# Optimization experiments

Hardware: AMD Instinct MI355X
Metric: run time of the kernel (lower is better)

## Reference

```python
import jax, jax.numpy as jnp
import numpy as np

L, H, E, V, BS = 12, 12, 768, 50257, 1024
HS = E // H
EPS = 1e-5


def _ln(x, w, b):
    m = jnp.mean(x, axis=-1, keepdims=True)
    v = jnp.mean(jnp.square(x - m), axis=-1, keepdims=True)
    return (x - m) * jax.lax.rsqrt(v + EPS) * w + b


def setup_inputs() -> dict:
    key = jax.random.key(0)
    ks = jax.random.split(key, 16)
    s = 0.02
    inp = {
        "idx": jax.random.randint(ks[0], (2, 1024), 0, V),
        "wte": jax.random.normal(ks[1], (V, E), jnp.float32) * s,
        "wpe": jax.random.normal(ks[2], (BS, E), jnp.float32) * s,
        "ln1_w": jnp.ones((L, E), jnp.float32),
        "ln1_b": jnp.zeros((L, E), jnp.float32),
        "attn_w": jax.random.normal(ks[3], (L, E, 3 * E), jnp.float32) * s,
        "attn_b": jnp.zeros((L, 3 * E), jnp.float32),
        "proj_w": jax.random.normal(ks[4], (L, E, E), jnp.float32) * s,
        "proj_b": jnp.zeros((L, E), jnp.float32),
        "ln2_w": jnp.ones((L, E), jnp.float32),
        "ln2_b": jnp.zeros((L, E), jnp.float32),
        "fc_w": jax.random.normal(ks[5], (L, E, 4 * E), jnp.float32) * s,
        "fc_b": jnp.zeros((L, 4 * E), jnp.float32),
        "fcp_w": jax.random.normal(ks[6], (L, 4 * E, E), jnp.float32) * s,
        "fcp_b": jnp.zeros((L, E), jnp.float32),
        "lnf_w": jnp.ones((E,), jnp.float32),
        "lnf_b": jnp.zeros((E,), jnp.float32),
    }
    return inp


def _gpt_forward(idx, wte, wpe, ln1_w, ln1_b, attn_w, attn_b, proj_w, proj_b,
                 ln2_w, ln2_b, fc_w, fc_b, fcp_w, fcp_b, lnf_w, lnf_b):
    B, T = idx.shape
    x = wte[idx] + wpe[:T]  # [B,T,E]
    causal = jnp.tril(jnp.ones((T, T), bool))
    scale = 1.0 / np.sqrt(HS)

    def block(x, p):
        (l1w, l1b, aw, ab, pw, pb, l2w, l2b, fw, fb, pww, pwb) = p
        qkv = _ln(x, l1w, l1b) @ aw + ab  # [B,T,3E]
        q, k, v = jnp.split(qkv, 3, axis=-1)
        q = q.reshape(B, T, H, HS).transpose(0, 2, 1, 3)  # [B,H,T,hs]
        k = k.reshape(B, T, H, HS).transpose(0, 2, 1, 3)
        v = v.reshape(B, T, H, HS).transpose(0, 2, 1, 3)
        att = jnp.einsum('bhqd,bhkd->bhqk', q, k) * scale
        att = jnp.where(causal, att, -jnp.inf)
        att = jax.nn.softmax(att, axis=-1)
        y = jnp.einsum('bhqk,bhkd->bhqd', att, v)
        y = y.transpose(0, 2, 1, 3).reshape(B, T, E)
        x = x + y @ pw + pb
        h = jax.nn.gelu(_ln(x, l2w, l2b) @ fw + fb, approximate=False)
        x = x + h @ pww + pwb
        return x, None

    params = (ln1_w, ln1_b, attn_w, attn_b, proj_w, proj_b,
              ln2_w, ln2_b, fc_w, fc_b, fcp_w, fcp_b)
    x, _ = jax.lax.scan(block, x, params)
    x = _ln(x, lnf_w, lnf_b)
    return x @ wte.T  # tied lm_head, training-mode full logits [B,T,V]


def reference(idx, wte, wpe, ln1_w, ln1_b, attn_w, attn_b, proj_w, proj_b,
              ln2_w, ln2_b, fc_w, fc_b, fcp_w, fcp_b, lnf_w, lnf_b):
    return _gpt_forward(idx, wte, wpe, ln1_w, ln1_b, attn_w, attn_b, proj_w,
                        proj_b, ln2_w, ln2_b, fc_w, fc_b, fcp_w, fcp_b,
                        lnf_w, lnf_b)
```

## Files before the change

kernel.cpp:

```cpp
#include <hip/hip_runtime.h>
#include <hip/hip_bf16.h>


typedef __bf16 bf16x8 __attribute__((ext_vector_type(8)));
typedef float f32x4 __attribute__((ext_vector_type(4)));
typedef unsigned int u32x4 __attribute__((ext_vector_type(4)));
typedef unsigned short ushort_t;

__device__ inline unsigned short f2bf(float f) {
    unsigned int u = __float_as_uint(f);
    u += 0x7FFFu + ((u >> 16) & 1u);
    return (unsigned short)(u >> 16);
}
__device__ inline unsigned int pk2(float a, float b) {
    return (unsigned int)f2bf(a) | ((unsigned int)f2bf(b) << 16);
}
__device__ inline float gelu_f(float v) {
    return 0.5f * v * (1.0f + erff(v * 0.70710678118654752f));
}
__device__ inline void gld16(const ushort_t* g, ushort_t* l) {
    __builtin_amdgcn_global_load_lds(
        (const __attribute__((address_space(1))) void*)g,
        (__attribute__((address_space(3))) void*)l, 16, 0, 0);
}
__device__ inline void store_c(float* p, float v) { *p = v; }
__device__ inline void store_c(ushort_t* p, float v) { *p = f2bf(v); }

__global__ __launch_bounds__(192) void embed_kernel(
    const int* __restrict__ idx, const float* __restrict__ wte,
    const float* __restrict__ wpe, float* __restrict__ x) {
    int row = blockIdx.x;
    int t = row & 1023;
    int tok = idx[row];
    const float4* src = (const float4*)(wte + (size_t)tok * 768);
    const float4* pe  = (const float4*)(wpe + (size_t)t * 768);
    float4* dst = (float4*)(x + (size_t)row * 768);
    int i = threadIdx.x;
    float4 a = src[i], b = pe[i];
    float4 r; r.x = a.x + b.x; r.y = a.y + b.y; r.z = a.z + b.z; r.w = a.w + b.w;
    dst[i] = r;
}

__global__ __launch_bounds__(256) void ln_kernel(
    const float* __restrict__ in, const float* __restrict__ w,
    const float* __restrict__ b, ushort_t* __restrict__ out) {
    int row = blockIdx.x;
    const float* r = in + (size_t)row * 768;
    int tid = threadIdx.x;
    float v[3];
#pragma unroll
    for (int j = 0; j < 3; j++) v[j] = r[tid + j * 256];
    float s = v[0] + v[1] + v[2];
    __shared__ float sh1[4], sh2[4];
#pragma unroll
    for (int o = 32; o; o >>= 1) s += __shfl_down(s, o);
    if ((tid & 63) == 0) sh1[tid >> 6] = s;
    __syncthreads();
    float mean = (sh1[0] + sh1[1] + sh1[2] + sh1[3]) * (1.0f / 768.0f);
    float d0 = v[0] - mean, d1 = v[1] - mean, d2 = v[2] - mean;
    float sq = d0 * d0 + d1 * d1 + d2 * d2;
#pragma unroll
    for (int o = 32; o; o >>= 1) sq += __shfl_down(sq, o);
    if ((tid & 63) == 0) sh2[tid >> 6] = sq;
    __syncthreads();
    float var = (sh2[0] + sh2[1] + sh2[2] + sh2[3]) * (1.0f / 768.0f);
    float rstd = rsqrtf(var + 1e-5f);
#pragma unroll
    for (int j = 0; j < 3; j++) {
        int c = tid + j * 256;
        out[(size_t)row * 768 + c] = f2bf((v[j] - mean) * rstd * w[c] + b[c]);
    }
}

__global__ __launch_bounds__(256) void transpose_all(
    const float* __restrict__ aw, const float* __restrict__ pw,
    const float* __restrict__ fw, const float* __restrict__ fpw,
    ushort_t* __restrict__ awT, ushort_t* __restrict__ pwT,
    ushort_t* __restrict__ fwT, ushort_t* __restrict__ fpwT) {
    int t = blockIdx.x;
    const float* in; ushort_t* out; int N, K, n0, k0;
    if (t < 432)       { in = aw;  out = awT;  N = 2304; K = 768;
                         n0 = (t % 36) * 64; k0 = (t / 36) * 64; }
    else if (t < 576)  { t -= 432;  in = pw;  out = pwT;  N = 768;  K = 768;
                         n0 = (t % 12) * 64; k0 = (t / 12) * 64; }
    else if (t < 1152) { t -= 576;  in = fw;  out = fwT;  N = 3072; K = 768;
                         n0 = (t % 48) * 64; k0 = (t / 48) * 64; }
    else               { t -= 1152; in = fpw; out = fpwT; N = 768;  K = 3072;
                         n0 = (t % 12) * 64; k0 = (t / 12) * 64; }
    __shared__ float tl[64][65];
    int tid = threadIdx.x;
    int r = tid >> 4, c = (tid & 15) * 4;
#pragma unroll
    for (int j = 0; j < 4; j++) {
        float4 v = *(const float4*)(in + (size_t)(k0 + r + j * 16) * N + n0 + c);
        tl[r + j * 16][c] = v.x; tl[r + j * 16][c + 1] = v.y;
        tl[r + j * 16][c + 2] = v.z; tl[r + j * 16][c + 3] = v.w;
    }
    __syncthreads();
    int nr = tid >> 2, kc = (tid & 3) * 16;
    unsigned int u[8];
#pragma unroll
    for (int j = 0; j < 8; j++)
        u[j] = pk2(tl[kc + 2 * j][nr], tl[kc + 2 * j + 1][nr]);
    u32x4 a = {u[0], u[1], u[2], u[3]}, b = {u[4], u[5], u[6], u[7]};
    ushort_t* op = out + (size_t)(n0 + nr) * K + k0 + kc;
    *(u32x4*)op = a;
    *(u32x4*)(op + 8) = b;
}

__global__ __launch_bounds__(256) void convert_bf(
    const float* __restrict__ in, ushort_t* __restrict__ out, long long n8) {
    long long i = (long long)blockIdx.x * 256 + threadIdx.x;
    long long stride = (long long)gridDim.x * 256;
    for (; i < n8; i += stride) {
        const float4* s = (const float4*)(in + i * 8);
        float4 a = s[0], b = s[1];
        u32x4 u = {pk2(a.x, a.y), pk2(a.z, a.w), pk2(b.x, b.y), pk2(b.z, b.w)};
        *(u32x4*)(out + i * 8) = u;
    }
}

__global__ __launch_bounds__(256) void vtrans_kernel(
    const ushort_t* __restrict__ qkvb, ushort_t* __restrict__ vt) {
    int t0 = blockIdx.x * 64;
    int z = blockIdx.y;
    int b = z / 12, hh = z % 12;
    const ushort_t* src = qkvb + (size_t)b * 1024 * 2304 + 1536 + hh * 64;
    ushort_t* dst = vt + (size_t)z * 64 * 1024;
    __shared__ __align__(16) ushort_t tl[64][72];
    int tid = threadIdx.x;
    int r = tid >> 2, c = (tid & 3) * 16;
    const ushort_t* sp = src + (size_t)(t0 + r) * 2304 + c;
    u32x4 v0 = *(const u32x4*)sp;
    u32x4 v1 = *(const u32x4*)(sp + 8);
    *(u32x4*)&tl[r][c] = v0;
    *(u32x4*)&tl[r][c + 8] = v1;
    __syncthreads();
    int f = tid >> 2, tc = (tid & 3) * 16;
    unsigned int u[8];
#pragma unroll
    for (int j = 0; j < 8; j++)
        u[j] = (unsigned int)tl[tc + 2 * j][f] | ((unsigned int)tl[tc + 2 * j + 1][f] << 16);
    u32x4 a = {u[0], u[1], u[2], u[3]}, b2 = {u[4], u[5], u[6], u[7]};
    ushort_t* op = dst + (size_t)f * 1024 + t0 + tc;
    *(u32x4*)op = a;
    *(u32x4*)(op + 8) = b2;
}

__global__ __launch_bounds__(256) void attn_kernel(
    const ushort_t* __restrict__ qkvb,
    const ushort_t* __restrict__ vt,
    ushort_t* __restrict__ y) {
    int qt = (int)gridDim.x - 1 - (int)blockIdx.x;
    int q0 = qt * 128;
    int z = blockIdx.y;
    int b = z / 12, h = z % 12;

    __shared__ __align__(16) ushort_t Ks[64 * 64];
    __shared__ __align__(16) ushort_t Vs[64 * 64];
    __shared__ __align__(16) ushort_t Ps[4][32 * 72];

    int tid = threadIdx.x;
    int lane = tid & 63, w = tid >> 6;
    int fr = lane & 15;
    int g4 = lane >> 4;
    int kg = g4 * 8;

    const ushort_t* qbase = qkvb + (size_t)b * 1024 * 2304;
    bf16x8 qf[2][2];
#pragma unroll
    for (int m = 0; m < 2; m++)
#pragma unroll
        for (int ks = 0; ks < 2; ks++)
            qf[m][ks] = *(const bf16x8*)(qbase +
                (size_t)(q0 + w * 32 + m * 16 + fr) * 2304 + h * 64 + ks * 32 + kg);

    f32x4 oacc[2][4] = {};
    float mrow[2][4], lrow[2][4];
#pragma unroll
    for (int m = 0; m < 2; m++)
#pragma unroll
        for (int i = 0; i < 4; i++) { mrow[m][i] = -1e30f; lrow[m][i] = 0.f; }

    const ushort_t* vtb = vt + (size_t)z * 64 * 1024;
    int nkt = ((q0 + 127) >> 6) + 1;
    const float LOG2E = 1.4426950408889634f;
    const float sc = 0.125f;
    int swr = (fr & 7) << 3;

    for (int kt = 0; kt < nkt; kt++) {
        int k0 = kt << 6;
#pragma unroll
        for (int c2 = 0; c2 < 2; c2++) {
            int c = tid + c2 * 256;
            int row = c >> 3;
            int col8 = ((c & 7) << 3) ^ ((row & 7) << 3);
            gld16(qbase + (size_t)(k0 + row) * 2304 + 768 + h * 64 + col8, Ks + c * 8);
            gld16(vtb + (size_t)row * 1024 + k0 + col8, Vs + c * 8);
        }
        __syncthreads();
        bool active = (k0 <= q0 + w * 32 + 31);
        if (active) {
            f32x4 s[2][4] = {};
#pragma unroll
            for (int ks = 0; ks < 2; ks++) {
                int cc = (ks * 32 + kg) ^ swr;
                bf16x8 kf[4];
#pragma unroll
                for (int n = 0; n < 4; n++)
                    kf[n] = *(const bf16x8*)(Ks + (n * 16 + fr) * 64 + cc);
#pragma unroll
                for (int m = 0; m < 2; m++)
#pragma unroll
                    for (int n = 0; n < 4; n++)
                        s[m][n] = __builtin_amdgcn_mfma_f32_16x16x32_bf16(qf[m][ks], kf[n], s[m][n], 0, 0, 0);
            }
            float al[2][4];
#pragma unroll
            for (int m = 0; m < 2; m++) {
#pragma unroll
                for (int i = 0; i < 4; i++) {
                    int q = q0 + w * 32 + m * 16 + g4 * 4 + i;
                    float pm = -1e30f;
#pragma unroll
                    for (int n = 0; n < 4; n++) {
                        int kv = k0 + n * 16 + fr;
                        float v = (kv <= q) ? s[m][n][i] * sc : -1e30f;
                        s[m][n][i] = v;
                        pm = fmaxf(pm, v);
                    }
                    pm = fmaxf(pm, __shfl_xor(pm, 1));
                    pm = fmaxf(pm, __shfl_xor(pm, 2));
                    pm = fmaxf(pm, __shfl_xor(pm, 4));
                    pm = fmaxf(pm, __shfl_xor(pm, 8));
                    float mn = fmaxf(mrow[m][i], pm);
                    float alpha = __builtin_exp2f((mrow[m][i] - mn) * LOG2E);
                    mrow[m][i] = mn;
                    al[m][i] = alpha;
                    float ps = 0.f;
#pragma unroll
                    for (int n = 0; n < 4; n++) {
                        float pv = __builtin_exp2f((s[m][n][i] - mn) * LOG2E);
                        s[m][n][i] = pv;
                        ps += pv;
                    }
                    ps += __shfl_xor(ps, 1);
                    ps += __shfl_xor(ps, 2);
                    ps += __shfl_xor(ps, 4);
                    ps += __shfl_xor(ps, 8);
                    lrow[m][i] = lrow[m][i] * alpha + ps;
                }
            }
#pragma unroll
            for (int m = 0; m < 2; m++)
#pragma unroll
                for (int nd = 0; nd < 4; nd++)
#pragma unroll
                    for (int i = 0; i < 4; i++)
                        oacc[m][nd][i] *= al[m][i];
#pragma unroll
            for (int m = 0; m < 2; m++)
#pragma unroll
                for (int n = 0; n < 4; n++)
#pragma unroll
                    for (int i = 0; i < 4; i++)
                        Ps[w][(m * 16 + g4 * 4 + i) * 72 + n * 16 + fr] = f2bf(s[m][n][i]);
        }
        __syncthreads();
        if (active) {
#pragma unroll
            for (int ks = 0; ks < 2; ks++) {
                int cc = (ks * 32 + kg) ^ swr;
                bf16x8 pa[2], vf[4];
#pragma unroll
                for (int m = 0; m < 2; m++)
                    pa[m] = *(const bf16x8*)(&Ps[w][(m * 16 + fr) * 72 + ks * 32 + kg]);
#pragma unroll
                for (int nd = 0; nd < 4; nd++)
                    vf[nd] = *(const bf16x8*)(Vs + (nd * 16 + fr) * 64 + cc);
#pragma unroll
                for (int m = 0; m < 2; m++)
#pragma unroll
                    for (int nd = 0; nd < 4; nd++)
                        oacc[m][nd] = __builtin_amdgcn_mfma_f32_16x16x32_bf16(pa[m], vf[nd], oacc[m][nd], 0, 0, 0);
            }
        }
        __syncthreads();
    }
    ushort_t* yb = y + (size_t)b * 1024 * 768 + h * 64;
#pragma unroll
    for (int m = 0; m < 2; m++)
#pragma unroll
        for (int nd = 0; nd < 4; nd++)
#pragma unroll
            for (int i = 0; i < 4; i++) {
                int q = q0 + w * 32 + m * 16 + g4 * 4 + i;
                yb[(size_t)q * 768 + nd * 16 + fr] = f2bf(oacc[m][nd][i] / lrow[m][i]);
            }
}

template <int BM, int EPI, typename TC>
__global__ __launch_bounds__(256) void gemm2(
    const ushort_t* __restrict__ A, int lda,
    const ushort_t* __restrict__ B, int ldb,
    TC* __restrict__ C, int ldc,
    const float* __restrict__ bias, const float* __restrict__ R,
    int M, int N, int K) {
    constexpr int MR = BM / 32;
    int brow = blockIdx.y * BM;
    int bcol = blockIdx.x * 128;

    __shared__ __align__(16) ushort_t As[BM * 64];
    __shared__ __align__(16) ushort_t Bs[128 * 64];

    int tid = threadIdx.x;
    int lane = tid & 63, wid = tid >> 6;
    int wr = (wid >> 1) * (BM / 2);
    int wc = (wid & 1) * 64;
    int fr = lane & 15;
    int g4 = lane >> 4;
    int kg = g4 * 8;
    int swr = (fr & 7) << 3;

    int colk = ((tid & 7) << 3) ^ (((tid >> 3) & 7) << 3);
    const ushort_t* Agr[MR];
    const ushort_t* Bgr[4];
#pragma unroll
    for (int rg = 0; rg < MR; rg++)
        Agr[rg] = A + (size_t)(brow + rg * 32 + (tid >> 3)) * lda + colk;
#pragma unroll
    for (int rg = 0; rg < 4; rg++) {
        int br = bcol + rg * 32 + (tid >> 3);
        if (br > N - 1) br = N - 1;
        Bgr[rg] = B + (size_t)br * ldb + colk;
    }
    ushort_t* Al = As + tid * 8;
    ushort_t* Bl = Bs + tid * 8;

    f32x4 acc[MR][4] = {};

    for (int k0 = 0; k0 < K; k0 += 64) {
#pragma unroll
        for (int rg = 0; rg < MR; rg++) gld16(Agr[rg] + k0, Al + rg * 2048);
#pragma unroll
        for (int rg = 0; rg < 4; rg++) gld16(Bgr[rg] + k0, Bl + rg * 2048);
        __syncthreads();
#pragma unroll
        for (int ks = 0; ks < 2; ks++) {
            int cc = (ks * 32 + kg) ^ swr;
            bf16x8 af[MR], bfv[4];
#pragma unroll
            for (int m = 0; m < MR; m++)
                af[m] = *(const bf16x8*)(As + (wr + m * 16 + fr) * 64 + cc);
#pragma unroll
            for (int n = 0; n < 4; n++)
                bfv[n] = *(const bf16x8*)(Bs + (wc + n * 16 + fr) * 64 + cc);
#pragma unroll
            for (int m = 0; m < MR; m++)
#pragma unroll
                for (int n = 0; n < 4; n++)
                    acc[m][n] = __builtin_amdgcn_mfma_f32_16x16x32_bf16(af[m], bfv[n], acc[m][n], 0, 0, 0);
        }
        __syncthreads();
    }

    int cr = g4 * 4;
#pragma unroll
    for (int m = 0; m < MR; m++) {
#pragma unroll
        for (int n = 0; n < 4; n++) {
            int col = bcol + wc + n * 16 + fr;
            if (col < N) {
                float bv = bias ? bias[col] : 0.0f;
#pragma unroll
                for (int i = 0; i < 4; i++) {
                    int row = brow + wr + m * 16 + cr + i;
                    float v = acc[m][n][i] + bv;
                    if constexpr (EPI == 1) v = gelu_f(v);
                    if constexpr (EPI == 2) v += R[(size_t)row * ldc + col];
                    store_c(&C[(size_t)row * ldc + col], v);
                }
            }
        }
    }
}

__global__ __launch_bounds__(512, 1) void gemm256(
    const ushort_t* __restrict__ A, int lda,
    const ushort_t* __restrict__ B, int ldb,
    float* __restrict__ C, int ldc,
    int M, int N, int K) {
    int Rt = gridDim.x, P = gridDim.y;
    int wgid = blockIdx.x + Rt * blockIdx.y;
    int full = P >> 3;
    int thresh = full * 8 * Rt;
    int r, pp;
    if (wgid < thresh) {
        int g = wgid / (8 * Rt);
        int wi = wgid - g * (8 * Rt);
        r = wi >> 3;
        pp = g * 8 + (wi & 7);
    } else {
        int off = wgid - thresh;
        pp = full * 8 + off / Rt;
        r = off - (off / Rt) * Rt;
    }
    int brow = r * 256;
    int bcol = pp * 256;

    __shared__ __align__(16) ushort_t As[2][256 * 64];
    __shared__ __align__(16) ushort_t Bs[2][256 * 64];

    int tid = threadIdx.x;
    int lane = tid & 63, wid = tid >> 6;
    int wr = (wid >> 2) * 128;
    int wc = (wid & 3) * 64;
    int fr = lane & 15;
    int g4 = lane >> 4;
    int kg = g4 * 8;
    int swr = (fr & 7) << 3;

    int srow = tid >> 3;
    int scol = ((tid & 7) << 3) ^ ((srow & 7) << 3);
    const ushort_t* Ag[4];
    const ushort_t* Bg[4];
#pragma unroll
    for (int s = 0; s < 4; s++) {
        Ag[s] = A + (size_t)(brow + s * 64 + srow) * lda + scol;
        int br = bcol + s * 64 + srow;
        if (br > N - 1) br = N - 1;
        Bg[s] = B + (size_t)br * ldb + scol;
    }

    f32x4 acc[8][4] = {};
    int nt = K >> 6;

#pragma unroll
    for (int s = 0; s < 4; s++) {
        gld16(Ag[s], &As[0][s * 4096 + tid * 8]);
        gld16(Bg[s], &Bs[0][s * 4096 + tid * 8]);
    }

    for (int t = 0; t < nt; t++) {
        int cur = t & 1;
        if (t + 1 < nt) {
            int nxt = cur ^ 1;
            int k0 = (t + 1) << 6;
#pragma unroll
            for (int s = 0; s < 4; s++) {
                gld16(Ag[s] + k0, &As[nxt][s * 4096 + tid * 8]);
                gld16(Bg[s] + k0, &Bs[nxt][s * 4096 + tid * 8]);
            }
            asm volatile("s_waitcnt vmcnt(8)" ::: "memory");
        } else {
            asm volatile("s_waitcnt vmcnt(0)" ::: "memory");
        }
        __builtin_amdgcn_sched_barrier(0);
        __builtin_amdgcn_s_barrier();
        __builtin_amdgcn_sched_barrier(0);

        const ushort_t* Ab = &As[cur][0];
        const ushort_t* Bb = &Bs[cur][0];
#pragma unroll
        for (int ks = 0; ks < 2; ks++) {
            int cc = (ks * 32 + kg) ^ swr;
            bf16x8 af[8], bfv[4];
#pragma unroll
            for (int m = 0; m < 8; m++)
                af[m] = *(const bf16x8*)(Ab + (wr + m * 16 + fr) * 64 + cc);
#pragma unroll
            for (int n = 0; n < 4; n++)
                bfv[n] = *(const bf16x8*)(Bb + (wc + n * 16 + fr) * 64 + cc);
#pragma unroll
            for (int m = 0; m < 8; m++)
#pragma unroll
                for (int n = 0; n < 4; n++)
                    acc[m][n] = __builtin_amdgcn_mfma_f32_16x16x32_bf16(af[m], bfv[n], acc[m][n], 0, 0, 0);
        }
        asm volatile("s_waitcnt lgkmcnt(0)" ::: "memory");
        __builtin_amdgcn_sched_barrier(0);
        __builtin_amdgcn_s_barrier();
        __builtin_amdgcn_sched_barrier(0);
    }

    int cr = g4 * 4;
#pragma unroll
    for (int m = 0; m < 8; m++) {
#pragma unroll
        for (int n = 0; n < 4; n++) {
            int col = bcol + wc + n * 16 + fr;
            if (col < N) {
#pragma unroll
                for (int i = 0; i < 4; i++) {
                    int row = brow + wr + m * 16 + cr + i;
                    C[(size_t)row * ldc + col] = acc[m][n][i];
                }
            }
        }
    }
}

extern "C" void kernel_launch(void* const* d_in, const int* in_sizes, int n_in,
                              void* d_out, int out_size, void* d_ws, size_t ws_size,
                              hipStream_t stream) {
    const int*   idx    = (const int*)d_in[0];
    const float* wte    = (const float*)d_in[1];
    const float* wpe    = (const float*)d_in[2];
    const float* ln1_w  = (const float*)d_in[3];
    const float* ln1_b  = (const float*)d_in[4];
    const float* attn_w = (const float*)d_in[5];
    const float* attn_b = (const float*)d_in[6];
    const float* proj_w = (const float*)d_in[7];
    const float* proj_b = (const float*)d_in[8];
    const float* ln2_w  = (const float*)d_in[9];
    const float* ln2_b  = (const float*)d_in[10];
    const float* fc_w   = (const float*)d_in[11];
    const float* fc_b   = (const float*)d_in[12];
    const float* fcp_w  = (const float*)d_in[13];
    const float* fcp_b  = (const float*)d_in[14];
    const float* lnf_w  = (const float*)d_in[15];
    const float* lnf_b  = (const float*)d_in[16];
    float* out = (float*)d_out;

    char* p = (char*)d_ws;
    float*    x    = (float*)p;    p += (size_t)2048 * 768 * 4;
    ushort_t* xn   = (ushort_t*)p; p += (size_t)2048 * 768 * 2;
    ushort_t* qkvb = (ushort_t*)p; p += (size_t)2048 * 2304 * 2;
    ushort_t* y    = (ushort_t*)p; p += (size_t)2048 * 768 * 2;
    ushort_t* h    = (ushort_t*)p; p += (size_t)2048 * 3072 * 2;
    ushort_t* vt   = (ushort_t*)p; p += (size_t)24 * 64 * 1024 * 2;
    ushort_t* wteb = (ushort_t*)p; p += (size_t)50257 * 768 * 2;
    ushort_t* awT  = (ushort_t*)p; p += (size_t)2304 * 768 * 2;
    ushort_t* pwT  = (ushort_t*)p; p += (size_t)768 * 768 * 2;
    ushort_t* fwT  = (ushort_t*)p; p += (size_t)3072 * 768 * 2;
    ushort_t* fpwT = (ushort_t*)p; p += (size_t)768 * 3072 * 2;

    embed_kernel<<<2048, 192, 0, stream>>>(idx, wte, wpe, x);

    for (int l = 0; l < 12; l++) {
        ln_kernel<<<2048, 256, 0, stream>>>(x, ln1_w + l * 768, ln1_b + l * 768, xn);
        transpose_all<<<1728, 256, 0, stream>>>(
            attn_w + (size_t)l * 768 * 2304, proj_w + (size_t)l * 768 * 768,
            fc_w + (size_t)l * 768 * 3072, fcp_w + (size_t)l * 3072 * 768,
            awT, pwT, fwT, fpwT);
        gemm2<128, 0, ushort_t><<<dim3(18, 16), 256, 0, stream>>>(
            xn, 768, awT, 768, qkvb, 2304,
            attn_b + l * 2304, nullptr, 2048, 2304, 768);
        vtrans_kernel<<<dim3(16, 24), 256, 0, stream>>>(qkvb, vt);
        attn_kernel<<<dim3(8, 24), 256, 0, stream>>>(qkvb, vt, y);
        gemm2<64, 2, float><<<dim3(6, 32), 256, 0, stream>>>(
            y, 768, pwT, 768, x, 768,
            proj_b + l * 768, x, 2048, 768, 768);
        ln_kernel<<<2048, 256, 0, stream>>>(x, ln2_w + l * 768, ln2_b + l * 768, xn);
        gemm2<128, 1, ushort_t><<<dim3(24, 16), 256, 0, stream>>>(
            xn, 768, fwT, 768, h, 3072,
            fc_b + l * 3072, nullptr, 2048, 3072, 768);
        gemm2<64, 2, float><<<dim3(6, 32), 256, 0, stream>>>(
            h, 3072, fpwT, 3072, x, 768,
            fcp_b + l * 768, x, 2048, 768, 3072);
    }

    convert_bf<<<4096, 256, 0, stream>>>(wte, wteb, (50257LL * 768) / 8);
    ln_kernel<<<2048, 256, 0, stream>>>(x, lnf_w, lnf_b, xn);
    gemm256<<<dim3(8, 197), 512, 0, stream>>>(
        xn, 768, wteb, 768, out, 50257, 2048, 50257, 768);
}
```

Measured before the change: 2.591 ms.

## Hoist weight transposes out of layer loop and fuse V transpose into QKV GEMM

When the workspace is large enough, all 12 layers' weight transposes run in one batched launch before the layer loop instead of once per layer. The separate V-transpose kernel is removed: the QKV GEMM epilogue writes V columns directly in transposed layout to the vt buffer. This cuts per-layer launch overhead, at the cost of a larger workspace and scattered narrow stores in the epilogue.

```diff
diff --git a/kernel.cpp b/kernel.cpp
--- a/kernel.cpp
+++ b/kernel.cpp
@@ -5,6 +5,7 @@
 typedef __bf16 bf16x8 __attribute__((ext_vector_type(8)));
 typedef float f32x4 __attribute__((ext_vector_type(4)));
 typedef unsigned int u32x4 __attribute__((ext_vector_type(4)));
+typedef unsigned int u32x2 __attribute__((ext_vector_type(2)));
 typedef unsigned short ushort_t;
 
 __device__ inline unsigned short f2bf(float f) {
@@ -87,6 +88,8 @@
                          n0 = (t % 48) * 64; k0 = (t / 48) * 64; }
     else               { t -= 1152; in = fpw; out = fpwT; N = 768;  K = 3072;
                          n0 = (t % 12) * 64; k0 = (t / 12) * 64; }
+    size_t zo = (size_t)blockIdx.z * (size_t)K * (size_t)N;
+    in += zo; out += zo;
     __shared__ float tl[64][65];
     int tid = threadIdx.x;
     int r = tid >> 4, c = (tid & 15) * 4;
@@ -118,33 +121,6 @@
         u32x4 u = {pk2(a.x, a.y), pk2(a.z, a.w), pk2(b.x, b.y), pk2(b.z, b.w)};
         *(u32x4*)(out + i * 8) = u;
     }
-}
-
-__global__ __launch_bounds__(256) void vtrans_kernel(
-    const ushort_t* __restrict__ qkvb, ushort_t* __restrict__ vt) {
-    int t0 = blockIdx.x * 64;
-    int z = blockIdx.y;
-    int b = z / 12, hh = z % 12;
-    const ushort_t* src = qkvb + (size_t)b * 1024 * 2304 + 1536 + hh * 64;
-    ushort_t* dst = vt + (size_t)z * 64 * 1024;
-    __shared__ __align__(16) ushort_t tl[64][72];
-    int tid = threadIdx.x;
-    int r = tid >> 2, c = (tid & 3) * 16;
-    const ushort_t* sp = src + (size_t)(t0 + r) * 2304 + c;
-    u32x4 v0 = *(const u32x4*)sp;
-    u32x4 v1 = *(const u32x4*)(sp + 8);
-    *(u32x4*)&tl[r][c] = v0;
-    *(u32x4*)&tl[r][c + 8] = v1;
-    __syncthreads();
-    int f = tid >> 2, tc = (tid & 3) * 16;
-    unsigned int u[8];
-#pragma unroll
-    for (int j = 0; j < 8; j++)
-        u[j] = (unsigned int)tl[tc + 2 * j][f] | ((unsigned int)tl[tc + 2 * j + 1][f] << 16);
-    u32x4 a = {u[0], u[1], u[2], u[3]}, b2 = {u[4], u[5], u[6], u[7]};
-    ushort_t* op = dst + (size_t)f * 1024 + t0 + tc;
-    *(u32x4*)op = a;
-    *(u32x4*)(op + 8) = b2;
 }
 
 __global__ __launch_bounds__(256) void attn_kernel(
@@ -305,6 +281,7 @@
     const ushort_t* __restrict__ B, int ldb,
     TC* __restrict__ C, int ldc,
     const float* __restrict__ bias, const float* __restrict__ R,
+    ushort_t* __restrict__ VT,
     int M, int N, int K) {
     constexpr int MR = BM / 32;
     int brow = blockIdx.y * BM;
@@ -372,6 +349,18 @@
             int col = bcol + wc + n * 16 + fr;
             if (col < N) {
                 float bv = bias ? bias[col] : 0.0f;
+                if constexpr (EPI == 3) {
+                    if (col >= 1536) {
+                        int d = col - 1536;
+                        int h2 = d >> 6, dd = d & 63;
+                        int row0 = brow + wr + m * 16 + cr;
+                        int bb = row0 >> 10, t0 = row0 & 1023;
+                        u32x2 val = {pk2(acc[m][n][0] + bv, acc[m][n][1] + bv),
+                                     pk2(acc[m][n][2] + bv, acc[m][n][3] + bv)};
+                        *(u32x2*)(VT + ((size_t)(bb * 12 + h2) * 64 + dd) * 1024 + t0) = val;
+                        continue;
+                    }
+                }
 #pragma unroll
                 for (int i = 0; i < 4; i++) {
                     int row = brow + wr + m * 16 + cr + i;
@@ -522,6 +511,10 @@
     const float* lnf_b  = (const float*)d_in[16];
     float* out = (float*)d_out;
 
+    const size_t S_AW = (size_t)2304 * 768, S_PW = (size_t)768 * 768;
+    const size_t S_FW = (size_t)3072 * 768, S_FPW = (size_t)768 * 3072;
+    const size_t S_L = S_AW + S_PW + S_FW + S_FPW;
+
     char* p = (char*)d_ws;
     float*    x    = (float*)p;    p += (size_t)2048 * 768 * 4;
     ushort_t* xn   = (ushort_t*)p; p += (size_t)2048 * 768 * 2;
@@ -529,35 +522,47 @@
     ushort_t* y    = (ushort_t*)p; p += (size_t)2048 * 768 * 2;
     ushort_t* h    = (ushort_t*)p; p += (size_t)2048 * 3072 * 2;
     ushort_t* vt   = (ushort_t*)p; p += (size_t)24 * 64 * 1024 * 2;
-    ushort_t* wteb = (ushort_t*)p; p += (size_t)50257 * 768 * 2;
-    ushort_t* awT  = (ushort_t*)p; p += (size_t)2304 * 768 * 2;
-    ushort_t* pwT  = (ushort_t*)p; p += (size_t)768 * 768 * 2;
-    ushort_t* fwT  = (ushort_t*)p; p += (size_t)3072 * 768 * 2;
-    ushort_t* fpwT = (ushort_t*)p; p += (size_t)768 * 3072 * 2;
+    ushort_t* wT   = (ushort_t*)p;
+
+    bool allT = ws_size >= (size_t)(37748736 + 12 * S_L * 2 + 1024);
+    ushort_t *awT, *pwT, *fwT, *fpwT, *wteb;
+    size_t oA, oP, oF, oFP;
+    if (allT) {
+        awT = wT; pwT = awT + 12 * S_AW; fwT = pwT + 12 * S_PW; fpwT = fwT + 12 * S_FW;
+        oA = S_AW; oP = S_PW; oF = S_FW; oFP = S_FPW;
+        wteb = wT;
+    } else {
+        awT = wT; pwT = awT + S_AW; fwT = pwT + S_PW; fpwT = fwT + S_FW;
+        oA = oP = oF = oFP = 0;
+        wteb = fpwT + S_FPW;
+    }
 
     embed_kernel<<<2048, 192, 0, stream>>>(idx, wte, wpe, x);
+    if (allT)
+        transpose_all<<<dim3(1728, 1, 12), 256, 0, stream>>>(
+            attn_w, proj_w, fc_w, fcp_w, awT, pwT, fwT, fpwT);
 
     for (int l = 0; l < 12; l++) {
         ln_kernel<<<2048, 256, 0, stream>>>(x, ln1_w + l * 768, ln1_b + l * 768, xn);
-        transpose_all<<<1728, 256, 0, stream>>>(
-            attn_w + (size_t)l * 768 * 2304, proj_w + (size_t)l * 768 * 768,
-            fc_w + (size_t)l * 768 * 3072, fcp_w + (size_t)l * 3072 * 768,
-            awT, pwT, fwT, fpwT);
-        gemm2<128, 0, ushort_t><<<dim3(18, 16), 256, 0, stream>>>(
-            xn, 768, awT, 768, qkvb, 2304,
-            attn_b + l * 2304, nullptr, 2048, 2304, 768);
-        vtrans_kernel<<<dim3(16, 24), 256, 0, stream>>>(qkvb, vt);
+        if (!allT)
+            transpose_all<<<dim3(1728, 1, 1), 256, 0, stream>>>(
+                attn_w + (size_t)l * S_AW, proj_w + (size_t)l * S_PW,
+                fc_w + (size_t)l * S_FW, fcp_w + (size_t)l * S_FPW,
+                awT, pwT, fwT, fpwT);
+        gemm2<128, 3, ushort_t><<<dim3(18, 16), 256, 0, stream>>>(
+            xn, 768, awT + l * oA, 768, qkvb, 2304,
+            attn_b + l * 2304, nullptr, vt, 2048, 2304, 768);
         attn_kernel<<<dim3(8, 24), 256, 0, stream>>>(qkvb, vt, y);
         gemm2<64, 2, float><<<dim3(6, 32), 256, 0, stream>>>(
-            y, 768, pwT, 768, x, 768,
-            proj_b + l * 768, x, 2048, 768, 768);
+            y, 768, pwT + l * oP, 768, x, 768,
+            proj_b + l * 768, x, nullptr, 2048, 768, 768);
         ln_kernel<<<2048, 256, 0, stream>>>(x, ln2_w + l * 768, ln2_b + l * 768, xn);
         gemm2<128, 1, ushort_t><<<dim3(24, 16), 256, 0, stream>>>(
-            xn, 768, fwT, 768, h, 3072,
-            fc_b + l * 3072, nullptr, 2048, 3072, 768);
+            xn, 768, fwT + l * oF, 768, h, 3072,
+            fc_b + l * 3072, nullptr, nullptr, 2048, 3072, 768);
         gemm2<64, 2, float><<<dim3(6, 32), 256, 0, stream>>>(
-            h, 3072, fpwT, 3072, x, 768,
-            fcp_b + l * 768, x, 2048, 768, 3072);
+            h, 3072, fpwT + l * oFP, 3072, x, 768,
+            fcp_b + l * 768, x, nullptr, 2048, 768, 3072);
     }
 
     convert_bf<<<4096, 256, 0, stream>>>(wte, wteb, (50257LL * 768) / 8);
```

Measured after the change: 2.729 ms. 1.05x slower.
